# Kernel tuning notes

Hardware: AMD Instinct MI355X
Metric: run time of the kernel (lower is better)

The kernel has to match this reference:

```python
import jax, jax.numpy as jnp
import numpy as np

NUM_HEADS = 16
NUM_KV_HEADS = 8
HEAD_DIM = 128
EPS = 1e-6
SLIDING_WINDOW = 1024
ROPE_THETA = 10000.0


def _rms_norm(x, w):
    # per-head RMSNorm in fp32, as in Qwen3RMSNorm
    xf = x.astype(jnp.float32)
    var = jnp.mean(xf * xf, axis=-1, keepdims=True)
    return (w * (xf * jax.lax.rsqrt(var + EPS))).astype(x.dtype)


def _rotate_half(x):
    d = x.shape[-1] // 2
    return jnp.concatenate([-x[..., d:], x[..., :d]], axis=-1)


def setup_inputs() -> dict:
    key = jax.random.key(0)
    ks = jax.random.split(key, 6)
    B, S, H = 2, 2048, 2048
    hidden_states = jax.random.normal(ks[0], (B, S, H), dtype=jnp.float32)
    # RoPE tables per HF convention: cos/sin of shape [B, S, head_dim]
    inv_freq = 1.0 / (ROPE_THETA ** (np.arange(0, HEAD_DIM, 2, dtype=np.float32) / HEAD_DIM))
    pos = np.arange(S, dtype=np.float32)
    ang = np.outer(pos, inv_freq)  # [S, HEAD_DIM/2]
    emb = np.concatenate([ang, ang], axis=-1)  # [S, HEAD_DIM]
    cos = jnp.broadcast_to(jnp.asarray(np.cos(emb)), (B, S, HEAD_DIM))
    sin = jnp.broadcast_to(jnp.asarray(np.sin(emb)), (B, S, HEAD_DIM))
    sc = 0.02
    Wq = jax.random.normal(ks[1], (NUM_HEADS * HEAD_DIM, H), dtype=jnp.float32) * sc
    Wk = jax.random.normal(ks[2], (NUM_KV_HEADS * HEAD_DIM, H), dtype=jnp.float32) * sc
    Wv = jax.random.normal(ks[3], (NUM_KV_HEADS * HEAD_DIM, H), dtype=jnp.float32) * sc
    Wo = jax.random.normal(ks[4], (H, NUM_HEADS * HEAD_DIM), dtype=jnp.float32) * sc
    q_norm_w = jnp.ones((HEAD_DIM,), dtype=jnp.float32)
    k_norm_w = jnp.ones((HEAD_DIM,), dtype=jnp.float32)
    return {"hidden_states": hidden_states, "cos": cos, "sin": sin,
            "Wq": Wq, "Wk": Wk, "Wv": Wv, "Wo": Wo,
            "q_norm_w": q_norm_w, "k_norm_w": k_norm_w}


def reference(hidden_states, cos, sin, Wq, Wk, Wv, Wo, q_norm_w, k_norm_w):
    B, S, H = hidden_states.shape
    scaling = HEAD_DIM ** -0.5
    # projections (torch Linear: y = x @ W.T), reshape to [B, nH, S, D]
    q = jnp.einsum('bsh,oh->bso', hidden_states, Wq).reshape(B, S, NUM_HEADS, HEAD_DIM)
    k = jnp.einsum('bsh,oh->bso', hidden_states, Wk).reshape(B, S, NUM_KV_HEADS, HEAD_DIM)
    v = jnp.einsum('bsh,oh->bso', hidden_states, Wv).reshape(B, S, NUM_KV_HEADS, HEAD_DIM)
    q = _rms_norm(q, q_norm_w).transpose(0, 2, 1, 3)  # [B, nH, S, D]
    k = _rms_norm(k, k_norm_w).transpose(0, 2, 1, 3)  # [B, nKV, S, D]
    v = v.transpose(0, 2, 1, 3)
    # RoPE, cos/sin broadcast over heads (unsqueeze_dim=1)
    c = cos[:, None, :, :]
    s = sin[:, None, :, :]
    q = q * c + _rotate_half(q) * s
    k = k * c + _rotate_half(k) * s
    # GQA: repeat kv heads
    groups = NUM_HEADS // NUM_KV_HEADS
    k = jnp.repeat(k, groups, axis=1)
    v = jnp.repeat(v, groups, axis=1)
    # causal + sliding-window mask
    i = jnp.arange(S)[:, None]
    j = jnp.arange(S)[None, :]
    mask = (j <= i) & (i - j < SLIDING_WINDOW)  # [S, S]
    scores = jnp.einsum('bhqd,bhkd->bhqk', q, k) * scaling
    scores = jnp.where(mask[None, None], scores, jnp.finfo(scores.dtype).min)
    probs = jax.nn.softmax(scores, axis=-1)
    attn = jnp.einsum('bhqk,bhkd->bhqd', probs, v)  # [B, nH, S, D]
    attn = attn.transpose(0, 2, 1, 3).reshape(B, S, NUM_HEADS * HEAD_DIM)
    out = jnp.einsum('bso,ho->bsh', attn, Wo)
    return out
```

## Files before the change

### kernel.cpp

```cpp
#include <hip/hip_runtime.h>
#include <stdint.h>

#define S_LEN 2048
#define BATCH 2
#define HID 2048
#define NH 16
#define NKV 8
#define HD 128
#define WINDOW 1024
#define SCALE 0.08838834764831845f
#define QKVW 4096

typedef unsigned short u16;
typedef unsigned int u32;
typedef __attribute__((ext_vector_type(8))) short short8;
typedef __attribute__((ext_vector_type(4))) float f32x4;
typedef __attribute__((ext_vector_type(16))) float f32x16;
typedef __attribute__((ext_vector_type(4))) u16 u16x4;

__device__ __forceinline__ u16 f2b(float f) {
  u32 u = __builtin_bit_cast(u32, f);
  return (u16)((u + 0x7fffu + ((u >> 16) & 1u)) >> 16);
}
__device__ __forceinline__ float b2f(u16 h) {
  u32 u = ((u32)h) << 16;
  return __builtin_bit_cast(float, u);
}
__device__ __forceinline__ u32 pk_bf16(float a, float b) {
  u32 d;
  asm("v_cvt_pk_bf16_f32 %0, %1, %2" : "=v"(d) : "v"(a), "v"(b));
  return d;
}

__device__ __forceinline__ void gload_lds16(const u16* g, u16* l) {
  __builtin_amdgcn_global_load_lds(
      (const __attribute__((address_space(1))) u32*)g,
      (__attribute__((address_space(3))) u32*)l, 16, 0, 0);
}

template <int N>
__device__ __forceinline__ void wait_vm() {
  if constexpr (N == 0) asm volatile("s_waitcnt vmcnt(0)" ::: "memory");
  else if constexpr (N == 8) asm volatile("s_waitcnt vmcnt(8)" ::: "memory");
}

__global__ __launch_bounds__(256) void k_conv(const float* __restrict__ src,
                                              u16* __restrict__ dst, int n4) {
  int i = blockIdx.x * blockDim.x + threadIdx.x;
  int st = gridDim.x * blockDim.x;
  for (; i < n4; i += st) {
    f32x4 v = ((const f32x4*)src)[i];
    u16x4 o;
    o[0] = f2b(v[0]); o[1] = f2b(v[1]); o[2] = f2b(v[2]); o[3] = f2b(v[3]);
    ((u16x4*)dst)[i] = o;
  }
}

__device__ __forceinline__ void store_c(u16* C, long idx, float v) { C[idx] = f2b(v); }
__device__ __forceinline__ void store_c(float* C, long idx, float v) { C[idx] = v; }

template <typename OutT>
__global__ __launch_bounds__(256, 2) void k_gemm2b(const u16* __restrict__ A,
                                                   const u16* __restrict__ B,
                                                   OutT* __restrict__ C,
                                                   int M, int N, int K) {
  __shared__ u16 sA[2][128 * 64];
  __shared__ u16 sB[2][128 * 64];
  const int tid = threadIdx.x;
  const int lane = tid & 63;
  const int w = tid >> 6;
  const int l15 = lane & 15;
  const int lg = lane >> 4;
  const int wm = w >> 1;
  const int wn = w & 1;
  const int sw = l15 & 7;

  const int gx = gridDim.x;
  const int nwg = gx * gridDim.y;
  const int flat = blockIdx.y * gx + blockIdx.x;
  const int tile = (flat & 7) * (nwg >> 3) + (flat >> 3);
  const long m0 = (long)(tile / gx) * 128;
  const long n0 = (long)(tile % gx) * 128;

  const u16* Abase = A + m0 * K;
  const u16* Bbase = B + n0 * K;

  int aOff[4], bOff[4], dstOff[4];
#pragma unroll
  for (int i = 0; i < 4; ++i) {
    const int c = tid + i * 256;
    const int row = c >> 3, chs = c & 7;
    const int scol = (chs ^ (row & 7)) * 8;
    aOff[i] = row * K + scol;
    bOff[i] = row * K + scol;
    dstOff[i] = c * 8;
  }

  f32x4 acc[4][4];
  const f32x4 z4 = {0.f, 0.f, 0.f, 0.f};
#pragma unroll
  for (int i = 0; i < 4; ++i)
#pragma unroll
    for (int j = 0; j < 4; ++j) acc[i][j] = z4;

  const int arow = (wm * 64 + l15) * 64;
  const int brow = (wn * 64 + l15) * 64;
  const int akc0 = (lg ^ sw) * 8;
  const int akc1 = ((4 + lg) ^ sw) * 8;

  const int NT = K >> 6;

#define STG(KT, BUF)                                                     \
  _Pragma("unroll") for (int i_ = 0; i_ < 4; ++i_)                       \
      gload_lds16(Abase + aOff[i_] + (KT) * 64, &sA[BUF][dstOff[i_]]);   \
  _Pragma("unroll") for (int i_ = 0; i_ < 4; ++i_)                       \
      gload_lds16(Bbase + bOff[i_] + (KT) * 64, &sB[BUF][dstOff[i_]]);

  STG(0, 0)

  for (int t = 0; t < NT; ++t) {
    const int cur = t & 1;
    if (t + 1 < NT) {
      STG(t + 1, cur ^ 1)
      wait_vm<8>();
    } else {
      wait_vm<0>();
    }
    __builtin_amdgcn_sched_barrier(0);
    __builtin_amdgcn_s_barrier();
    __builtin_amdgcn_sched_barrier(0);

#pragma unroll
    for (int kk = 0; kk < 2; ++kk) {
      const int akc = (kk == 0) ? akc0 : akc1;
      short8 afk[4], bfk[4];
#pragma unroll
      for (int i = 0; i < 4; ++i)
        afk[i] = *(const short8*)&sA[cur][arow + i * 16 * 64 + akc];
#pragma unroll
      for (int j = 0; j < 4; ++j)
        bfk[j] = *(const short8*)&sB[cur][brow + j * 16 * 64 + akc];
      __builtin_amdgcn_s_setprio(1);
#pragma unroll
      for (int i = 0; i < 4; ++i)
#pragma unroll
        for (int j = 0; j < 4; ++j)
          acc[i][j] = __builtin_amdgcn_mfma_f32_16x16x32_bf16(
              afk[i], bfk[j], acc[i][j], 0, 0, 0);
      __builtin_amdgcn_s_setprio(0);
    }
    __builtin_amdgcn_s_barrier();
    __builtin_amdgcn_sched_barrier(0);
  }
#undef STG

#pragma unroll
  for (int i = 0; i < 4; ++i)
#pragma unroll
    for (int j = 0; j < 4; ++j)
#pragma unroll
      for (int r = 0; r < 4; ++r) {
        long row = m0 + wm * 64 + i * 16 + lg * 4 + r;
        long col = n0 + wn * 64 + j * 16 + l15;
        store_c(C, row * (long)N + col, acc[i][j][r]);
      }
}

__global__ __launch_bounds__(256) void k_normrope(u16* __restrict__ QKV,
                                                  const float* __restrict__ cosb,
                                                  const float* __restrict__ sinb,
                                                  const float* __restrict__ qw,
                                                  const float* __restrict__ kw) {
  const int lane = threadIdx.x & 63;
  const int w = threadIdx.x >> 6;
  int row = blockIdx.x * 4 + w;
  const int nQ = BATCH * S_LEN * NH;
  u16* p;
  const float* nw;
  int tok;
  float sc;
  if (row < nQ) {
    tok = row >> 4;
    int h = row & 15;
    p = QKV + (long)tok * QKVW + h * HD;
    nw = qw;
    sc = SCALE;
  } else {
    int r2 = row - nQ;
    tok = r2 >> 3;
    int h = r2 & 7;
    p = QKV + (long)tok * QKVW + 2048 + h * HD;
    nw = kw;
    sc = 1.0f;
  }
  float x0 = b2f(p[lane]);
  float x1 = b2f(p[lane + 64]);
  float ss = x0 * x0 + x1 * x1;
#pragma unroll
  for (int mk = 1; mk < 64; mk <<= 1) ss += __shfl_xor(ss, mk, 64);
  float rinv = rsqrtf(ss * (1.0f / 128.0f) + 1e-6f);
  float y0 = x0 * rinv * nw[lane];
  float y1 = x1 * rinv * nw[lane + 64];
  const float* cp = cosb + (long)tok * HD;
  const float* sp = sinb + (long)tok * HD;
  float o0 = (y0 * cp[lane] - y1 * sp[lane]) * sc;
  float o1 = (y1 * cp[lane + 64] + y0 * sp[lane + 64]) * sc;
  p[lane] = f2b(o0);
  p[lane + 64] = f2b(o1);
}

__global__ __launch_bounds__(256, 2) void k_attn(const u16* __restrict__ QKV,
                                                 u16* __restrict__ AO) {
  __shared__ u16 sK[64 * 128];
  __shared__ u16 sVT[64 * 128];
  const int tid = threadIdx.x;
  const int lane = tid & 63;
  const int l31 = lane & 31;
  const int hi = lane >> 5;
  const int w = tid >> 6;
  const int q0 = blockIdx.x * 128;
  const int h = blockIdx.y;
  const int b = blockIdx.z;
  const int kvh = h >> 1;
  const int qw0 = q0 + w * 32;
  const int iq = qw0 + l31;

  const long tokbase = (long)b * S_LEN;
  const u16* Qrow = QKV + (tokbase + qw0 + l31) * QKVW + h * HD;
  short8 qf[8];
#pragma unroll
  for (int dt = 0; dt < 8; ++dt) qf[dt] = *(const short8*)(Qrow + dt * 16 + hi * 8);

  f32x16 o[4];
#pragma unroll
  for (int n = 0; n < 4; ++n)
#pragma unroll
    for (int r = 0; r < 16; ++r) o[n][r] = 0.f;
  float m = 0.f, lsum = 0.f;

  const u16* Kbase = QKV + tokbase * QKVW + 2048 + kvh * HD;
  const u16* Vbase = QKV + tokbase * QKVW + 3072 + kvh * HD;

  int kc_row[4], kc_off[4];
  u16* kc_dst[4];
#pragma unroll
  for (int i = 0; i < 4; ++i) {
    const int c = tid + 256 * i;
    kc_row[i] = c >> 4;
    kc_off[i] = (((c & 15) ^ ((c >> 4) & 7))) * 8;
    kc_dst[i] = &sK[c * 8];
  }
  const int rp = tid & 31;
  const int dc0 = tid >> 5;
  const int rg_st = rp >> 2;

  int t_lo = q0 - (WINDOW - 1);
  t_lo = (t_lo < 0 ? 0 : t_lo) >> 6;
  const int t_hi = (q0 + 127) >> 6;

  for (int t = t_lo; t <= t_hi; ++t) {
    const int kv0 = t << 6;
#pragma unroll
    for (int i = 0; i < 4; ++i)
      gload_lds16(Kbase + (long)(kv0 + kc_row[i]) * QKVW + kc_off[i], kc_dst[i]);
#pragma unroll
    for (int i = 0; i < 2; ++i) {
      const int dc = dc0 + i * 8;
      const u16* vp = Vbase + (long)(kv0 + 2 * rp) * QKVW + dc * 8;
      short8 v0 = *(const short8*)vp;
      short8 v1 = *(const short8*)(vp + QKVW);
#pragma unroll
      for (int e = 0; e < 8; ++e) {
        const int d = dc * 8 + e;
        const int unit = d * 8 + (rg_st ^ (d & 7));
        ((u32*)sVT)[unit * 4 + (rp & 3)] = (u32)(u16)v0[e] | ((u32)(u16)v1[e] << 16);
      }
    }
    __syncthreads();

    const bool skipw = (kv0 > qw0 + 31) || (kv0 + 63 < qw0 - (WINDOW - 1));
    if (!skipw) {
      const bool full = (kv0 + 63 <= qw0) && ((qw0 + 31) - kv0 < WINDOW);
      f32x16 s0, s1;
#pragma unroll
      for (int r = 0; r < 16; ++r) { s0[r] = 0.f; s1[r] = 0.f; }
      const int rsw = l31 & 7;
#pragma unroll
      for (int dt = 0; dt < 8; ++dt) {
        const int ch = hi + 2 * dt;
        const short8 kf0 = *(const short8*)&sK[(l31 * 16 + (ch ^ rsw)) * 8];
        s0 = __builtin_amdgcn_mfma_f32_32x32x16_bf16(kf0, qf[dt], s0, 0, 0, 0);
        const short8 kf1 = *(const short8*)&sK[((l31 + 32) * 16 + (ch ^ rsw)) * 8];
        s1 = __builtin_amdgcn_mfma_f32_32x32x16_bf16(kf1, qf[dt], s1, 0, 0, 0);
      }
      float p[32];
#pragma unroll
      for (int r = 0; r < 16; ++r) { p[r] = s0[r]; p[16 + r] = s1[r]; }
      if (!full) {
#pragma unroll
        for (int r = 0; r < 32; ++r) {
          const int kk = kv0 + (r >> 4) * 32 + 4 * hi + (r & 3) + 8 * ((r >> 2) & 3);
          p[r] = ((u32)(iq - kk) < (u32)WINDOW) ? p[r] : -3.0e38f;
        }
      }
      float tm = p[0];
#pragma unroll
      for (int r = 1; r < 32; ++r) tm = fmaxf(tm, p[r]);
      tm = fmaxf(tm, __shfl_xor(tm, 32, 64));
      const float mn = fmaxf(m, tm);
      const float al = __expf(m - mn);
      m = mn;
      float rs = 0.f;
#pragma unroll
      for (int r = 0; r < 32; ++r) { p[r] = __expf(p[r] - mn); rs += p[r]; }
      rs += __shfl_xor(rs, 32, 64);
      lsum = lsum * al + rs;
#pragma unroll
      for (int n = 0; n < 4; ++n)
#pragma unroll
        for (int r = 0; r < 16; ++r) o[n][r] *= al;

      short8 pf[4];
#pragma unroll
      for (int ks = 0; ks < 4; ++ks) {
        const int bb = (ks >> 1) * 16 + (ks & 1) * 8;
        u32 a0 = pk_bf16(p[bb + 0], p[bb + 1]);
        u32 b0 = pk_bf16(p[bb + 4], p[bb + 5]);
        u32 a1 = pk_bf16(p[bb + 2], p[bb + 3]);
        u32 b1 = pk_bf16(p[bb + 6], p[bb + 7]);
        asm volatile("v_permlane32_swap_b32 %0, %1" : "+v"(a0), "+v"(b0));
        asm volatile("v_permlane32_swap_b32 %0, %1" : "+v"(a1), "+v"(b1));
        union { u32 u[4]; short8 s; } uu;
        uu.u[0] = a0; uu.u[1] = a1; uu.u[2] = b0; uu.u[3] = b1;
        pf[ks] = uu.s;
      }
#pragma unroll
      for (int dt = 0; dt < 4; ++dt) {
        const int d = l31 + 32 * dt;
        const int dsw = d & 7;
#pragma unroll
        for (int ks = 0; ks < 4; ++ks) {
          const int rg = ks * 2 + hi;
          const short8 vf = *(const short8*)&sVT[(d * 8 + (rg ^ dsw)) * 8];
          o[dt] = __builtin_amdgcn_mfma_f32_32x32x16_bf16(vf, pf[ks], o[dt], 0, 0, 0);
        }
      }
    }
    __syncthreads();
  }

  __syncthreads();
  float* R = ((float*)sK) + w * 1024;
  const float rl = 1.0f / lsum;
  const int half = hi;
#pragma unroll
  for (int dt = 0; dt < 4; ++dt) {
#pragma unroll
    for (int r = 0; r < 16; ++r) {
      const int dp = 4 * hi + (r & 3) + 8 * (r >> 2);
      R[dp * 32 + (l31 ^ (4 * (dp & 7)))] = o[dt][r] * rl;
    }
    __syncthreads();
    union { u16 hh[16]; short8 s[2]; } U;
#pragma unroll
    for (int j = 0; j < 16; ++j) {
      const int dp = half * 16 + j;
      U.hh[j] = f2b(R[dp * 32 + (l31 ^ (4 * (dp & 7)))]);
    }
    u16* dst = AO + (tokbase + q0 + w * 32 + l31) * (NH * HD) + h * HD + dt * 32 + half * 16;
    *(short8*)dst = U.s[0];
    *(short8*)(dst + 8) = U.s[1];
    __syncthreads();
  }
}

extern "C" void kernel_launch(void* const* d_in, const int* in_sizes, int n_in,
                              void* d_out, int out_size, void* d_ws, size_t ws_size,
                              hipStream_t stream) {
  const float* hs   = (const float*)d_in[0];
  const float* cosb = (const float*)d_in[1];
  const float* sinb = (const float*)d_in[2];
  const float* Wq   = (const float*)d_in[3];
  const float* Wk   = (const float*)d_in[4];
  const float* Wv   = (const float*)d_in[5];
  const float* Wo   = (const float*)d_in[6];
  const float* qw   = (const float*)d_in[7];
  const float* kw   = (const float*)d_in[8];
  float* out = (float*)d_out;

  const long SZ_X  = (long)BATCH * S_LEN * HID;
  const long SZ_WQ = (long)NH * HD * HID;
  const long SZ_WK = (long)NKV * HD * HID;
  u16* Xb   = (u16*)d_ws;
  u16* Wqb  = Xb + SZ_X;
  u16* Wkb  = Wqb + SZ_WQ;
  u16* Wvb  = Wkb + SZ_WK;
  u16* Wob  = Wvb + SZ_WK;
  u16* QKVb = Wob + SZ_WQ;
  u16* AOb  = QKVb + (long)BATCH * S_LEN * QKVW;

  k_conv<<<2048, 256, 0, stream>>>(hs, Xb, (int)(SZ_X / 4));
  k_conv<<<1024, 256, 0, stream>>>(Wq, Wqb, (int)(SZ_WQ / 4));
  k_conv<<<512, 256, 0, stream>>>(Wk, Wkb, (int)(SZ_WK / 4));
  k_conv<<<512, 256, 0, stream>>>(Wv, Wvb, (int)(SZ_WK / 4));
  k_conv<<<1024, 256, 0, stream>>>(Wo, Wob, (int)(SZ_WQ / 4));

  k_gemm2b<u16><<<dim3(32, 32), 256, 0, stream>>>(
      Xb, Wqb, QKVb, BATCH * S_LEN, QKVW, HID);

  k_normrope<<<(BATCH * S_LEN * (NH + NKV)) / 4, 256, 0, stream>>>(QKVb, cosb, sinb, qw, kw);

  k_attn<<<dim3(S_LEN / 128, NH, BATCH), 256, 0, stream>>>(QKVb, AOb);

  k_gemm2b<float><<<dim3(16, 32), 256, 0, stream>>>(
      AOb, Wob, out, BATCH * S_LEN, HID, HID);
}
```

Measured before the change: 213.6 us.

## Add 128x256-tile GEMM kernel with K=32 stages for QKV projection

Adds a new bf16 MFMA GEMM kernel that uses 128x256 output tiles, with each wave owning a 128x64 slab, and a K-step of 32 double-buffered through direct global-to-LDS loads with an XOR swizzle. The QKV projection now launches this kernel on a 16x32 grid in place of the 128x128 k_gemm2b. The wider tile is meant to raise arithmetic intensity per LDS fetch and cut redundant A-tile loads. In exchange it uses more accumulator registers per thread (128 floats), runs half as many workgroups, and the shorter K step means more barriers per unit of work.

```diff
diff --git a/kernel.cpp b/kernel.cpp
--- a/kernel.cpp
+++ b/kernel.cpp
@@ -41,6 +41,7 @@
 template <int N>
 __device__ __forceinline__ void wait_vm() {
   if constexpr (N == 0) asm volatile("s_waitcnt vmcnt(0)" ::: "memory");
+  else if constexpr (N == 6) asm volatile("s_waitcnt vmcnt(6)" ::: "memory");
   else if constexpr (N == 8) asm volatile("s_waitcnt vmcnt(8)" ::: "memory");
 }
 
@@ -58,6 +59,110 @@
 
 __device__ __forceinline__ void store_c(u16* C, long idx, float v) { C[idx] = f2b(v); }
 __device__ __forceinline__ void store_c(float* C, long idx, float v) { C[idx] = v; }
+
+template <typename OutT>
+__global__ __launch_bounds__(256, 2) void k_gemmW(const u16* __restrict__ A,
+                                                  const u16* __restrict__ B,
+                                                  OutT* __restrict__ C,
+                                                  int M, int N, int K) {
+  __shared__ u16 sA[2][128 * 32];
+  __shared__ u16 sB[2][256 * 32];
+  const int tid = threadIdx.x;
+  const int lane = tid & 63;
+  const int w = tid >> 6;
+  const int l15 = lane & 15;
+  const int lg = lane >> 4;
+
+  const int gx = gridDim.x;
+  const int nwg = gx * gridDim.y;
+  const int flat = blockIdx.y * gx + blockIdx.x;
+  const int tile = (flat & 7) * (nwg >> 3) + (flat >> 3);
+  const long m0 = (long)(tile / gx) * 128;
+  const long n0 = (long)(tile % gx) * 256;
+
+  const u16* Abase = A + m0 * K;
+  const u16* Bbase = B + n0 * K;
+
+  int aOff[2], aDst[2], bOff[4], bDst[4];
+#pragma unroll
+  for (int i = 0; i < 2; ++i) {
+    const int c = tid + i * 256;
+    const int row = c >> 2, ch = c & 3;
+    aOff[i] = row * K + (ch ^ ((row >> 2) & 3)) * 8;
+    aDst[i] = c * 8;
+  }
+#pragma unroll
+  for (int i = 0; i < 4; ++i) {
+    const int c = tid + i * 256;
+    const int row = c >> 2, ch = c & 3;
+    bOff[i] = row * K + (ch ^ ((row >> 2) & 3)) * 8;
+    bDst[i] = c * 8;
+  }
+
+  f32x4 acc[8][4];
+  const f32x4 z4 = {0.f, 0.f, 0.f, 0.f};
+#pragma unroll
+  for (int i = 0; i < 8; ++i)
+#pragma unroll
+    for (int j = 0; j < 4; ++j) acc[i][j] = z4;
+
+  const int chsw = (lg ^ ((l15 >> 2) & 3)) * 8;
+  const int brow0 = w * 64;
+
+  const int NT = K >> 5;
+
+#define STG(KT, BUF)                                                    \
+  _Pragma("unroll") for (int i_ = 0; i_ < 2; ++i_)                      \
+      gload_lds16(Abase + aOff[i_] + (KT) * 32, &sA[BUF][aDst[i_]]);    \
+  _Pragma("unroll") for (int i_ = 0; i_ < 4; ++i_)                      \
+      gload_lds16(Bbase + bOff[i_] + (KT) * 32, &sB[BUF][bDst[i_]]);
+
+  STG(0, 0)
+
+  for (int t = 0; t < NT; ++t) {
+    const int cur = t & 1;
+    if (t + 1 < NT) {
+      STG(t + 1, cur ^ 1)
+      wait_vm<6>();
+    } else {
+      wait_vm<0>();
+    }
+    __builtin_amdgcn_sched_barrier(0);
+    __builtin_amdgcn_s_barrier();
+    __builtin_amdgcn_sched_barrier(0);
+
+    short8 af[8], bf[4];
+#pragma unroll
+    for (int i = 0; i < 8; ++i)
+      af[i] = *(const short8*)&sA[cur][(i * 16 + l15) * 32 + chsw];
+#pragma unroll
+    for (int j = 0; j < 4; ++j)
+      bf[j] = *(const short8*)&sB[cur][(brow0 + j * 16 + l15) * 32 + chsw];
+    __builtin_amdgcn_s_setprio(1);
+#pragma unroll
+    for (int i = 0; i < 8; ++i)
+#pragma unroll
+      for (int j = 0; j < 4; ++j)
+        acc[i][j] = __builtin_amdgcn_mfma_f32_16x16x32_bf16(
+            af[i], bf[j], acc[i][j], 0, 0, 0);
+    __builtin_amdgcn_s_setprio(0);
+
+    __builtin_amdgcn_s_barrier();
+    __builtin_amdgcn_sched_barrier(0);
+  }
+#undef STG
+
+#pragma unroll
+  for (int i = 0; i < 8; ++i)
+#pragma unroll
+    for (int j = 0; j < 4; ++j)
+#pragma unroll
+      for (int r = 0; r < 4; ++r) {
+        long row = m0 + i * 16 + lg * 4 + r;
+        long col = n0 + w * 64 + j * 16 + l15;
+        store_c(C, row * (long)N + col, acc[i][j][r]);
+      }
+}
 
 template <typename OutT>
 __global__ __launch_bounds__(256, 2) void k_gemm2b(const u16* __restrict__ A,
@@ -405,7 +510,7 @@
   k_conv<<<512, 256, 0, stream>>>(Wv, Wvb, (int)(SZ_WK / 4));
   k_conv<<<1024, 256, 0, stream>>>(Wo, Wob, (int)(SZ_WQ / 4));
 
-  k_gemm2b<u16><<<dim3(32, 32), 256, 0, stream>>>(
+  k_gemmW<u16><<<dim3(16, 32), 256, 0, stream>>>(
       Xb, Wqb, QKVb, BATCH * S_LEN, QKVW, HID);
 
   k_normrope<<<(BATCH * S_LEN * (NH + NKV)) / 4, 256, 0, stream>>>(QKVb, cosb, sinb, qw, kw);
```

Measured after the change: 211.0 us. No clear change (-1.2%).

## Fuse five fp32-to-bf16 conversions into one launch; single-buffer GEMM for occupancy

Applied to the files above, without the earlier changes.

Replaces the five separate conversion launches with one kernel that walks a concatenated index space and picks the source buffer by range, which removes launch overhead and tail effects. The GEMM drops its LDS double buffering and raises launch bounds to four blocks per CU, so it relies on more resident waves rather than in-block prefetch to hide load latency. The risk is that every k-step now waits for its own loads with no overlap inside a block, and the fused conversion adds a branch chain per element.

```diff
diff --git a/kernel.cpp b/kernel.cpp
--- a/kernel.cpp
+++ b/kernel.cpp
@@ -41,15 +41,29 @@
 template <int N>
 __device__ __forceinline__ void wait_vm() {
   if constexpr (N == 0) asm volatile("s_waitcnt vmcnt(0)" ::: "memory");
-  else if constexpr (N == 8) asm volatile("s_waitcnt vmcnt(8)" ::: "memory");
-}
-
-__global__ __launch_bounds__(256) void k_conv(const float* __restrict__ src,
-                                              u16* __restrict__ dst, int n4) {
+}
+
+#define CQ0 2097152
+#define CQ1 3145728
+#define CQ2 3670016
+#define CQ3 4194304
+#define CQ4 5242880
+__global__ __launch_bounds__(256) void k_conv5(const float* __restrict__ s0,
+                                               const float* __restrict__ s1,
+                                               const float* __restrict__ s2,
+                                               const float* __restrict__ s3,
+                                               const float* __restrict__ s4,
+                                               u16* __restrict__ dst) {
   int i = blockIdx.x * blockDim.x + threadIdx.x;
-  int st = gridDim.x * blockDim.x;
-  for (; i < n4; i += st) {
-    f32x4 v = ((const f32x4*)src)[i];
+  const int st = gridDim.x * blockDim.x;
+  for (; i < CQ4; i += st) {
+    const f32x4* src;
+    if (i < CQ0)      src = (const f32x4*)s0 + i;
+    else if (i < CQ1) src = (const f32x4*)s1 + (i - CQ0);
+    else if (i < CQ2) src = (const f32x4*)s2 + (i - CQ1);
+    else if (i < CQ3) src = (const f32x4*)s3 + (i - CQ2);
+    else              src = (const f32x4*)s4 + (i - CQ3);
+    f32x4 v = *src;
     u16x4 o;
     o[0] = f2b(v[0]); o[1] = f2b(v[1]); o[2] = f2b(v[2]); o[3] = f2b(v[3]);
     ((u16x4*)dst)[i] = o;
@@ -60,12 +74,12 @@
 __device__ __forceinline__ void store_c(float* C, long idx, float v) { C[idx] = v; }
 
 template <typename OutT>
-__global__ __launch_bounds__(256, 2) void k_gemm2b(const u16* __restrict__ A,
-                                                   const u16* __restrict__ B,
-                                                   OutT* __restrict__ C,
-                                                   int M, int N, int K) {
-  __shared__ u16 sA[2][128 * 64];
-  __shared__ u16 sB[2][128 * 64];
+__global__ __launch_bounds__(256, 4) void k_gemmS(const u16* __restrict__ A,
+                                                  const u16* __restrict__ B,
+                                                  OutT* __restrict__ C,
+                                                  int M, int N, int K) {
+  __shared__ u16 sA[128 * 64];
+  __shared__ u16 sB[128 * 64];
   const int tid = threadIdx.x;
   const int lane = tid & 63;
   const int w = tid >> 6;
@@ -110,22 +124,14 @@
 
   const int NT = K >> 6;
 
-#define STG(KT, BUF)                                                     \
-  _Pragma("unroll") for (int i_ = 0; i_ < 4; ++i_)                       \
-      gload_lds16(Abase + aOff[i_] + (KT) * 64, &sA[BUF][dstOff[i_]]);   \
-  _Pragma("unroll") for (int i_ = 0; i_ < 4; ++i_)                       \
-      gload_lds16(Bbase + bOff[i_] + (KT) * 64, &sB[BUF][dstOff[i_]]);
-
-  STG(0, 0)
-
   for (int t = 0; t < NT; ++t) {
-    const int cur = t & 1;
-    if (t + 1 < NT) {
-      STG(t + 1, cur ^ 1)
-      wait_vm<8>();
-    } else {
-      wait_vm<0>();
-    }
+#pragma unroll
+    for (int i = 0; i < 4; ++i)
+      gload_lds16(Abase + aOff[i] + t * 64, &sA[dstOff[i]]);
+#pragma unroll
+    for (int i = 0; i < 4; ++i)
+      gload_lds16(Bbase + bOff[i] + t * 64, &sB[dstOff[i]]);
+    wait_vm<0>();
     __builtin_amdgcn_sched_barrier(0);
     __builtin_amdgcn_s_barrier();
     __builtin_amdgcn_sched_barrier(0);
@@ -136,10 +142,10 @@
       short8 afk[4], bfk[4];
 #pragma unroll
       for (int i = 0; i < 4; ++i)
-        afk[i] = *(const short8*)&sA[cur][arow + i * 16 * 64 + akc];
+        afk[i] = *(const short8*)&sA[arow + i * 16 * 64 + akc];
 #pragma unroll
       for (int j = 0; j < 4; ++j)
-        bfk[j] = *(const short8*)&sB[cur][brow + j * 16 * 64 + akc];
+        bfk[j] = *(const short8*)&sB[brow + j * 16 * 64 + akc];
       __builtin_amdgcn_s_setprio(1);
 #pragma unroll
       for (int i = 0; i < 4; ++i)
@@ -152,7 +158,6 @@
     __builtin_amdgcn_s_barrier();
     __builtin_amdgcn_sched_barrier(0);
   }
-#undef STG
 
 #pragma unroll
   for (int i = 0; i < 4; ++i)
@@ -399,19 +404,15 @@
   u16* QKVb = Wob + SZ_WQ;
   u16* AOb  = QKVb + (long)BATCH * S_LEN * QKVW;
 
-  k_conv<<<2048, 256, 0, stream>>>(hs, Xb, (int)(SZ_X / 4));
-  k_conv<<<1024, 256, 0, stream>>>(Wq, Wqb, (int)(SZ_WQ / 4));
-  k_conv<<<512, 256, 0, stream>>>(Wk, Wkb, (int)(SZ_WK / 4));
-  k_conv<<<512, 256, 0, stream>>>(Wv, Wvb, (int)(SZ_WK / 4));
-  k_conv<<<1024, 256, 0, stream>>>(Wo, Wob, (int)(SZ_WQ / 4));
-
-  k_gemm2b<u16><<<dim3(32, 32), 256, 0, stream>>>(
+  k_conv5<<<2048, 256, 0, stream>>>(hs, Wq, Wk, Wv, Wo, Xb);
+
+  k_gemmS<u16><<<dim3(32, 32), 256, 0, stream>>>(
       Xb, Wqb, QKVb, BATCH * S_LEN, QKVW, HID);
 
   k_normrope<<<(BATCH * S_LEN * (NH + NKV)) / 4, 256, 0, stream>>>(QKVb, cosb, sinb, qw, kw);
 
   k_attn<<<dim3(S_LEN / 128, NH, BATCH), 256, 0, stream>>>(QKVb, AOb);
 
-  k_gemm2b<float><<<dim3(16, 32), 256, 0, stream>>>(
+  k_gemmS<float><<<dim3(16, 32), 256, 0, stream>>>(
       AOb, Wob, out, BATCH * S_LEN, HID, HID);
 }
```

After: 209.0 us. 1.02x faster.
